# Kernel optimization log

Hardware: AMD Instinct MI355X
Metric: run time of the kernel (lower is better)

The kernel has to match this reference:

```python
import jax, jax.numpy as jnp
import numpy as np

N, H, W, C = 8, 64, 64, 256  # C//4 = 64 query channels, HW = 4096 attention size


def setup_inputs() -> dict:
    key = jax.random.key(0)
    k1, k2, k3, k4 = jax.random.split(key, 4)
    src_mask = jax.random.uniform(k1, (N, H, W), dtype=jnp.float32)
    src_feature = jax.random.normal(k2, (N, H, W, C), dtype=jnp.float32)
    ref_feature = jax.random.normal(k3, (N, H, W, C), dtype=jnp.float32)
    w_query = jax.random.normal(k4, (C, C // 4), dtype=jnp.float32) * 0.02  # 1x1 conv weight
    return {"src_mask": src_mask, "src_feature": src_feature,
            "ref_feature": ref_feature, "w_query": w_query}


def _apply_attention_map(att_map, features):
    n, h, w, c = features.shape
    pixels = features.reshape(n, h * w, c).transpose(0, 2, 1)  # (N, C, HW)
    att_out = jnp.einsum('ncp,npq->ncq', pixels, att_map)      # (N, C, HW)
    return att_out.reshape(n, h, w, c)


def reference(src_mask, src_feature, ref_feature, w_query):
    n, h, w, c = src_feature.shape
    # 1x1 conv (no bias): per-pixel channel projection C -> C//4
    query = jnp.einsum('nhwc,cd->nhwd', src_feature, w_query).reshape(n, h * w, -1)
    # full (HW x HW) attention map, softmax over keys
    att_map = jax.nn.softmax(jnp.einsum('npd,nqd->npq', query, query), axis=-1)
    # original module applies the map to src_feature twice (src_att and ref_att)
    att_out = _apply_attention_map(att_map, src_feature)
    src_att = att_out
    ref_att = att_out
    m = src_mask[..., None]  # (N, H, W, 1)
    ex_guide_flow = m * ref_att + (1.0 - m) * ref_feature
    return jnp.concatenate([ex_guide_flow, src_att], axis=-1)  # (N, H, W, 2C)
```

## Files before the change

### kernel.cpp

```cpp
#include <hip/hip_runtime.h>

typedef unsigned short u16;
typedef unsigned int u32;
typedef __attribute__((ext_vector_type(8))) __bf16 bf16x8;
typedef __attribute__((ext_vector_type(8))) _Float16 f16x8;
typedef __attribute__((ext_vector_type(4))) float f32x4;

__device__ __forceinline__ float b2f(u16 b) {
    union { u32 u; float f; } v; v.u = ((u32)b) << 16; return v.f;
}
__device__ __forceinline__ u16 f2bf(float f) {
    union { float f; u32 u; } v; v.f = f;
    u32 u = v.u;
    return (u16)((u + 0x7fffu + ((u >> 16) & 1u)) >> 16);
}
__device__ __forceinline__ u16 f2h(float f) {
    _Float16 h = (_Float16)f;
    return __builtin_bit_cast(u16, h);
}
__device__ __forceinline__ bf16x8 ldg8b(const u16* p) {
    uint4 v = *(const uint4*)p;
    return __builtin_bit_cast(bf16x8, v);
}
__device__ __forceinline__ f16x8 ldg8h(const u16* p) {
    uint4 v = *(const uint4*)p;
    return __builtin_bit_cast(f16x8, v);
}
__device__ __forceinline__ f32x4 mfma_bf(bf16x8 a, bf16x8 b, f32x4 c) {
    return __builtin_amdgcn_mfma_f32_16x16x32_bf16(a, b, c, 0, 0, 0);
}
__device__ __forceinline__ f32x4 mfma_h(f16x8 a, f16x8 b, f32x4 c) {
    return __builtin_amdgcn_mfma_f32_16x16x32_f16(a, b, c, 0, 0, 0);
}
__device__ __forceinline__ void gld16(const u16* g, u16* l) {
    __builtin_amdgcn_global_load_lds(
        (const __attribute__((address_space(1))) u32*)g,
        (__attribute__((address_space(3))) u32*)l, 16, 0, 0);
}


__global__ void k0_wt(const float* __restrict__ Wq,
                      u16* __restrict__ Wthi, u16* __restrict__ Wtlo) {
    int idx = blockIdx.x * 256 + threadIdx.x;
    int c = idx >> 6, d = idx & 63;
    float w = Wq[idx];
    u16 hi = f2bf(w);
    float rem = w - b2f(hi);
    Wthi[d * 256 + c] = hi;
    Wtlo[d * 256 + c] = f2bf(rem);
}

__global__ __launch_bounds__(256) void k1_query(
    const float* __restrict__ F, const u16* __restrict__ Wthi,
    const u16* __restrict__ Wtlo, u16* __restrict__ Qh) {
    const int t = threadIdx.x;
    const int w = t >> 6, L = t & 63, lane16 = L & 15, quad = L >> 4;
    const int R0 = blockIdx.x * 64;
    const int row = R0 + w * 16 + lane16;
    const f32x4 z4 = {0.f, 0.f, 0.f, 0.f};
    f32x4 acc[4] = {z4, z4, z4, z4};
    union U8 { bf16x8 v; u16 s[8]; };
#pragma unroll
    for (int ks = 0; ks < 8; ++ks) {
        const float* fp = F + (size_t)row * 256 + ks * 32 + quad * 8;
        float4 x0 = *(const float4*)fp;
        float4 x1 = *(const float4*)(fp + 4);
        float xs[8] = {x0.x, x0.y, x0.z, x0.w, x1.x, x1.y, x1.z, x1.w};
        U8 ahi, alo;
#pragma unroll
        for (int j = 0; j < 8; ++j) {
            u16 h = f2bf(xs[j]);
            ahi.s[j] = h;
            alo.s[j] = f2bf(xs[j] - b2f(h));
        }
#pragma unroll
        for (int nt = 0; nt < 4; ++nt) {
            const int off = (nt * 16 + lane16) * 256 + ks * 32 + quad * 8;
            bf16x8 bh = ldg8b(Wthi + off);
            bf16x8 bl = ldg8b(Wtlo + off);
            acc[nt] = mfma_bf(ahi.v, bh, acc[nt]);
            acc[nt] = mfma_bf(alo.v, bh, acc[nt]);
            acc[nt] = mfma_bf(ahi.v, bl, acc[nt]);
        }
    }
    const int orow = R0 + w * 16 + quad * 4;
#pragma unroll
    for (int nt = 0; nt < 4; ++nt) {
        const int d = nt * 16 + lane16;
#pragma unroll
        for (int r = 0; r < 4; ++r) {
            const int p = orow + r;
            Qh[(size_t)p * 64 + (d ^ ((p & 7) << 3))] = f2h(acc[nt][r]);
        }
    }
}

__global__ __launch_bounds__(256) void k2_suminv(
    const u16* __restrict__ Q, float* __restrict__ inv_l) {
    const int t = threadIdx.x;
    const int w = t >> 6, L = t & 63, lane16 = L & 15, quad = L >> 4, l7 = lane16 & 7;
    const int bx = blockIdx.x;
    const int n = bx & 7, pb = bx >> 3;
    const int P0 = pb * 32;
    const u16* Qn = Q + (size_t)n * 4096 * 64;

    f16x8 ap[2][2];
#pragma unroll
    for (int st = 0; st < 2; ++st) {
        const int row = P0 + st * 16 + lane16;
        ap[st][0] = ldg8h(Qn + row * 64 + ((quad * 8) ^ (l7 * 8)));
        ap[st][1] = ldg8h(Qn + row * 64 + ((32 + quad * 8) ^ (l7 * 8)));
    }
    float sums[2][4];
#pragma unroll
    for (int st = 0; st < 2; ++st)
#pragma unroll
        for (int r = 0; r < 4; ++r) sums[st][r] = 0.f;

    const f32x4 z4 = {0.f, 0.f, 0.f, 0.f};
    for (int s = 0; s < 32; ++s) {
#pragma unroll
        for (int nt = 0; nt < 2; ++nt) {
            const int qr = w * 1024 + s * 32 + nt * 16 + lane16;
            f16x8 b0 = ldg8h(Qn + qr * 64 + ((quad * 8) ^ (l7 * 8)));
            f16x8 b1 = ldg8h(Qn + qr * 64 + ((32 + quad * 8) ^ (l7 * 8)));
#pragma unroll
            for (int st = 0; st < 2; ++st) {
                f32x4 z = z4;
                z = mfma_h(ap[st][0], b0, z);
                z = mfma_h(ap[st][1], b1, z);
                sums[st][0] += __expf(z[0]);
                sums[st][1] += __expf(z[1]);
                sums[st][2] += __expf(z[2]);
                sums[st][3] += __expf(z[3]);
            }
        }
    }
    __shared__ float red[4][32];
#pragma unroll
    for (int st = 0; st < 2; ++st)
#pragma unroll
        for (int r = 0; r < 4; ++r) {
            float v = sums[st][r];
            v += __shfl_xor(v, 1);
            v += __shfl_xor(v, 2);
            v += __shfl_xor(v, 4);
            v += __shfl_xor(v, 8);
            if (lane16 == 0) red[w][st * 16 + quad * 4 + r] = v;
        }
    __syncthreads();
    if (t < 32) {
        float tot = red[0][t] + red[1][t] + red[2][t] + red[3][t];
        inv_l[n * 4096 + P0 + t] = 1.0f / tot;
    }
}

__global__ __launch_bounds__(256) void k3_gt(
    const float* __restrict__ F, u16* __restrict__ Gt) {
    const int t = threadIdx.x;
    const int bx = blockIdx.x;
    const int n = bx >> 6, s = bx & 63;
    const int p0 = s * 64;
    __shared__ float tile[64][65];
    const float* Fn = F + (size_t)n * 4096 * 256;
    u16* Gn = Gt + (size_t)(n * 64 + s) * 16384;
#pragma unroll 1
    for (int ct = 0; ct < 4; ++ct) {
        const int c0 = ct * 64;
        if (ct > 0) __syncthreads();
#pragma unroll
        for (int k = 0; k < 16; ++k) {
            int idx = k * 256 + t;
            int r = idx >> 6, cc = idx & 63;
            tile[r][cc] = Fn[(size_t)(p0 + r) * 256 + c0 + cc];
        }
        __syncthreads();
#pragma unroll
        for (int k = 0; k < 2; ++k) {
            int u = k * 256 + t;
            int cc = u & 63, S = u >> 6;
            int G = S ^ (cc & 7);
            u16 v[8];
#pragma unroll
            for (int j = 0; j < 8; ++j) v[j] = f2bf(tile[G * 8 + j][cc]);
            uint4 pk;
            pk.x = (u32)v[0] | ((u32)v[1] << 16);
            pk.y = (u32)v[2] | ((u32)v[3] << 16);
            pk.z = (u32)v[4] | ((u32)v[5] << 16);
            pk.w = (u32)v[6] | ((u32)v[7] << 16);
            *(uint4*)&Gn[(c0 + cc) * 64 + S * 8] = pk;
        }
    }
}

__global__ __launch_bounds__(256, 2) void k4_attn(
    const u16* __restrict__ Q, const u16* __restrict__ Gt,
    const float* __restrict__ invl, const float* __restrict__ mask,
    const float* __restrict__ ref, float* __restrict__ out) {
    const int t = threadIdx.x;
    const int w = t >> 6, L = t & 63, lane16 = L & 15, quad = L >> 4, l7 = lane16 & 7;
    const int bx = blockIdx.x;
    const int n = bx & 7, qb = bx >> 3;
    const int q0 = qb << 6;

    __shared__ u16 sGt[16384];
    __shared__ u16 sQp[4096];
    __shared__ u16 sP[4096];

    const u16* Qn = Q + (size_t)n * 4096 * 64;
    const u16* Gtn = Gt + (size_t)n * 64 * 16384;
    const float* iln = invl + n * 4096;

    f16x8 bq[4][2];
#pragma unroll
    for (int qt = 0; qt < 4; ++qt) {
        const int row = q0 + qt * 16 + lane16;
        bq[qt][0] = ldg8h(Qn + row * 64 + ((quad * 8) ^ (l7 * 8)));
        bq[qt][1] = ldg8h(Qn + row * 64 + ((32 + quad * 8) ^ (l7 * 8)));
    }

    const int pl = w * 16 + lane16;
    const int sA0 = pl * 64 + ((quad * 8) ^ (l7 * 8));
    const int sA1 = pl * 64 + ((32 + quad * 8) ^ (l7 * 8));
    int wrP[4];
#pragma unroll
    for (int qt = 0; qt < 4; ++qt)
        wrP[qt] = (qt * 16 + lane16) * 64 +
                  ((w * 16 + 8 * (quad >> 1)) ^ (l7 * 8)) + 4 * (quad & 1);
    const int dl = L * 8;

    const f32x4 z4 = {0.f, 0.f, 0.f, 0.f};
    f32x4 acc[4][4];
#pragma unroll
    for (int a = 0; a < 4; ++a)
#pragma unroll
        for (int b = 0; b < 4; ++b) acc[a][b] = z4;

#pragma unroll
    for (int j = 0; j < 2; ++j) {
        const int c = w * 2 + j;
        gld16(Qn + c * 512 + dl, &sQp[c * 512]);
    }
    __syncthreads();

#pragma unroll 1
    for (int i = 0; i < 64; ++i) {
#pragma unroll
        for (int j = 0; j < 8; ++j) {
            const int c = w * 8 + j;
            gld16(Gtn + (size_t)i * 16384 + c * 512 + dl, &sGt[c * 512]);
        }
        {
            f16x8 a0 = ldg8h(&sQp[sA0]);
            f16x8 a1 = ldg8h(&sQp[sA1]);
            float4 il4 = *(const float4*)(iln + i * 64 + w * 16 + quad * 4);
#pragma unroll
            for (int qt = 0; qt < 4; ++qt) {
                f32x4 z = z4;
                z = mfma_h(a0, bq[qt][0], z);
                z = mfma_h(a1, bq[qt][1], z);
                ushort4 pk;
                pk.x = f2bf(__expf(z[0]) * il4.x);
                pk.y = f2bf(__expf(z[1]) * il4.y);
                pk.z = f2bf(__expf(z[2]) * il4.z);
                pk.w = f2bf(__expf(z[3]) * il4.w);
                *(ushort4*)&sP[wrP[qt]] = pk;
            }
        }
        __syncthreads();
        if (i + 1 < 64) {
#pragma unroll
            for (int j = 0; j < 2; ++j) {
                const int c = w * 2 + j;
                gld16(Qn + (size_t)(i + 1) * 4096 + c * 512 + dl, &sQp[c * 512]);
            }
        }
#pragma unroll
        for (int h = 0; h < 2; ++h) {
            bf16x8 af[4], bb[4];
#pragma unroll
            for (int m = 0; m < 4; ++m)
                af[m] = ldg8b(&sP[(m * 16 + lane16) * 64 + ((h * 32 + quad * 8) ^ (l7 * 8))]);
#pragma unroll
            for (int nt = 0; nt < 4; ++nt)
                bb[nt] = ldg8b(&sGt[(w * 64 + nt * 16 + lane16) * 64 +
                                    ((h * 32 + quad * 8) ^ (l7 * 8))]);
#pragma unroll
            for (int nt = 0; nt < 4; ++nt)
#pragma unroll
                for (int m = 0; m < 4; ++m)
                    acc[m][nt] = mfma_bf(af[m], bb[nt], acc[m][nt]);
        }
        __syncthreads();
    }

    const int tb = qb >> 2;
    const int cb = (qb & 3) * 64;
    const float* maskn = mask + n * 4096;
    const float* refn = ref + (size_t)n * 4096 * 256;
    float* outn = out + (size_t)n * 4096 * 512;
#pragma unroll
    for (int nt = 0; nt < 4; ++nt) {
        const int ch = w * 64 + nt * 16 + lane16;
        const int pixel = ch * 16 + tb;
        const float m = maskn[pixel];
#pragma unroll
        for (int mt = 0; mt < 4; ++mt) {
            const int c4 = cb + mt * 16 + quad * 4;
            float4 r4 = *(const float4*)(refn + (size_t)pixel * 256 + c4);
            float a0 = acc[mt][nt][0], a1 = acc[mt][nt][1];
            float a2 = acc[mt][nt][2], a3 = acc[mt][nt][3];
            float4 a4 = {a0, a1, a2, a3};
            float4 bl4 = {m * a0 + (1.f - m) * r4.x,
                          m * a1 + (1.f - m) * r4.y,
                          m * a2 + (1.f - m) * r4.z,
                          m * a3 + (1.f - m) * r4.w};
            *(float4*)(outn + (size_t)pixel * 512 + 256 + c4) = a4;
            *(float4*)(outn + (size_t)pixel * 512 + c4) = bl4;
        }
    }
}

extern "C" void kernel_launch(void* const* d_in, const int* in_sizes, int n_in,
                              void* d_out, int out_size, void* d_ws, size_t ws_size,
                              hipStream_t stream) {
    const float* mask = (const float*)d_in[0];
    const float* F    = (const float*)d_in[1];
    const float* ref  = (const float*)d_in[2];
    const float* Wq   = (const float*)d_in[3];
    float* out = (float*)d_out;
    char* ws = (char*)d_ws;

    u16*   Wthi = (u16*)ws;
    u16*   Wtlo = (u16*)(ws + 32768);
    u16*   Qh   = (u16*)(ws + 65536);
    float* invl = (float*)(ws + 65536 + 4194304);
    u16*   Gt   = (u16*)(ws + 65536 + 4194304 + 131072);

    k0_wt    <<<64,   256, 0, stream>>>(Wq, Wthi, Wtlo);
    k1_query <<<512,  256, 0, stream>>>(F, Wthi, Wtlo, Qh);
    k2_suminv<<<1024, 256, 0, stream>>>(Qh, invl);
    k3_gt    <<<512,  256, 0, stream>>>(F, Gt);
    k4_attn  <<<512,  256, 0, stream>>>(Qh, Gt, invl, mask, ref, out);
}
```

Measured before the change: 272.1 us.

## Load Gt and Q fragments directly into registers, double-buffer P in LDS

The attention kernel stops staging the Gt and Q tiles through shared memory with global_load_lds. Each wave now loads its own Gt B-fragments and the next step's Q A-fragments and inverse-sum values straight into registers, prefetching one step ahead. The P tile is double-buffered in LDS, so each iteration needs one barrier instead of two. This cuts LDS traffic and occupancy pressure but raises register use and exposes global-load latency on the Gt fragments, which are issued in the same iteration that consumes them.

```diff
diff --git a/kernel.cpp b/kernel.cpp
--- a/kernel.cpp
+++ b/kernel.cpp
@@ -31,11 +31,6 @@
 }
 __device__ __forceinline__ f32x4 mfma_h(f16x8 a, f16x8 b, f32x4 c) {
     return __builtin_amdgcn_mfma_f32_16x16x32_f16(a, b, c, 0, 0, 0);
-}
-__device__ __forceinline__ void gld16(const u16* g, u16* l) {
-    __builtin_amdgcn_global_load_lds(
-        (const __attribute__((address_space(1))) u32*)g,
-        (__attribute__((address_space(3))) u32*)l, 16, 0, 0);
 }
 
 
@@ -203,31 +198,31 @@
     const int n = bx & 7, qb = bx >> 3;
     const int q0 = qb << 6;
 
-    __shared__ u16 sGt[16384];
-    __shared__ u16 sQp[4096];
-    __shared__ u16 sP[4096];
+    __shared__ u16 sP[2][4096];
 
     const u16* Qn = Q + (size_t)n * 4096 * 64;
     const u16* Gtn = Gt + (size_t)n * 64 * 16384;
     const float* iln = invl + n * 4096;
 
+    const int o0 = (quad * 8) ^ (l7 * 8);
+
     f16x8 bq[4][2];
 #pragma unroll
     for (int qt = 0; qt < 4; ++qt) {
-        const int row = q0 + qt * 16 + lane16;
-        bq[qt][0] = ldg8h(Qn + row * 64 + ((quad * 8) ^ (l7 * 8)));
-        bq[qt][1] = ldg8h(Qn + row * 64 + ((32 + quad * 8) ^ (l7 * 8)));
-    }
-
-    const int pl = w * 16 + lane16;
-    const int sA0 = pl * 64 + ((quad * 8) ^ (l7 * 8));
-    const int sA1 = pl * 64 + ((32 + quad * 8) ^ (l7 * 8));
+        const u16* r = Qn + (q0 + qt * 16 + lane16) * 64;
+        bq[qt][0] = ldg8h(r + o0);
+        bq[qt][1] = ldg8h(r + (o0 ^ 32));
+    }
+
+    const u16* qrow = Qn + (w * 16 + lane16) * 64;
+    const u16* grow = Gtn + (w * 64 + lane16) * 64;
+    const float* ilp = iln + w * 16 + quad * 4;
+
     int wrP[4];
 #pragma unroll
     for (int qt = 0; qt < 4; ++qt)
         wrP[qt] = (qt * 16 + lane16) * 64 +
                   ((w * 16 + 8 * (quad >> 1)) ^ (l7 * 8)) + 4 * (quad & 1);
-    const int dl = L * 8;
 
     const f32x4 z4 = {0.f, 0.f, 0.f, 0.f};
     f32x4 acc[4][4];
@@ -236,63 +231,71 @@
 #pragma unroll
         for (int b = 0; b < 4; ++b) acc[a][b] = z4;
 
-#pragma unroll
-    for (int j = 0; j < 2; ++j) {
-        const int c = w * 2 + j;
-        gld16(Qn + c * 512 + dl, &sQp[c * 512]);
-    }
-    __syncthreads();
+    f16x8 qa0[2], qa1[2];
+    float4 il[2];
+    bf16x8 gb[8];
+
+#define LOADSTEP(slot, step) do {                       \
+        const u16* _q = qrow + (step) * 4096;           \
+        qa0[slot] = ldg8h(_q + o0);                     \
+        qa1[slot] = ldg8h(_q + (o0 ^ 32));              \
+        il[slot] = *(const float4*)(ilp + (step) * 64); \
+    } while (0)
+
+#define LOADGB(step) do {                                   \
+        const u16* _g = grow + (size_t)(step) * 16384;      \
+        _Pragma("unroll")                                   \
+        for (int nt = 0; nt < 4; ++nt) {                    \
+            gb[nt * 2 + 0] = ldg8b(_g + nt * 1024 + o0);    \
+            gb[nt * 2 + 1] = ldg8b(_g + nt * 1024 + (o0 ^ 32)); \
+        }                                                   \
+    } while (0)
+
+#define ITER(i, cur, nxt) do {                                        \
+        LOADGB(i);                                                    \
+        if ((i) + 1 < 64) LOADSTEP(nxt, (i) + 1);                     \
+        {                   \
+            f16x8 a0 = qa0[cur], a1 = qa1[cur];                       \
+            float4 il4 = il[cur];                                     \
+            _Pragma("unroll")                                         \
+            for (int qt = 0; qt < 4; ++qt) {                          \
+                f32x4 z = z4;                                         \
+                z = mfma_h(a0, bq[qt][0], z);                         \
+                z = mfma_h(a1, bq[qt][1], z);                         \
+                ushort4 pk;                                           \
+                pk.x = f2bf(__expf(z[0]) * il4.x);                    \
+                pk.y = f2bf(__expf(z[1]) * il4.y);                    \
+                pk.z = f2bf(__expf(z[2]) * il4.z);                    \
+                pk.w = f2bf(__expf(z[3]) * il4.w);                    \
+                *(ushort4*)&sP[(i) & 1][wrP[qt]] = pk;                \
+            }                                                         \
+        }                                                             \
+        asm volatile("s_waitcnt lgkmcnt(0)\n\ts_barrier" ::: "memory"); \
+        _Pragma("unroll")                                             \
+        for (int h = 0; h < 2; ++h) {                   \
+            bf16x8 af[4];                                             \
+            _Pragma("unroll")                                         \
+            for (int m = 0; m < 4; ++m)                               \
+                af[m] = ldg8b(&sP[(i) & 1][(m * 16 + lane16) * 64 + (o0 ^ (h * 32))]); \
+            _Pragma("unroll")                                         \
+            for (int nt = 0; nt < 4; ++nt) {                          \
+                _Pragma("unroll")                                     \
+                for (int m = 0; m < 4; ++m)                           \
+                    acc[m][nt] = mfma_bf(af[m], gb[nt * 2 + h], acc[m][nt]); \
+            }                                                         \
+        }                                                             \
+    } while (0)
+
+    LOADSTEP(0, 0);
 
 #pragma unroll 1
-    for (int i = 0; i < 64; ++i) {
-#pragma unroll
-        for (int j = 0; j < 8; ++j) {
-            const int c = w * 8 + j;
-            gld16(Gtn + (size_t)i * 16384 + c * 512 + dl, &sGt[c * 512]);
-        }
-        {
-            f16x8 a0 = ldg8h(&sQp[sA0]);
-            f16x8 a1 = ldg8h(&sQp[sA1]);
-            float4 il4 = *(const float4*)(iln + i * 64 + w * 16 + quad * 4);
-#pragma unroll
-            for (int qt = 0; qt < 4; ++qt) {
-                f32x4 z = z4;
-                z = mfma_h(a0, bq[qt][0], z);
-                z = mfma_h(a1, bq[qt][1], z);
-                ushort4 pk;
-                pk.x = f2bf(__expf(z[0]) * il4.x);
-                pk.y = f2bf(__expf(z[1]) * il4.y);
-                pk.z = f2bf(__expf(z[2]) * il4.z);
-                pk.w = f2bf(__expf(z[3]) * il4.w);
-                *(ushort4*)&sP[wrP[qt]] = pk;
-            }
-        }
-        __syncthreads();
-        if (i + 1 < 64) {
-#pragma unroll
-            for (int j = 0; j < 2; ++j) {
-                const int c = w * 2 + j;
-                gld16(Qn + (size_t)(i + 1) * 4096 + c * 512 + dl, &sQp[c * 512]);
-            }
-        }
-#pragma unroll
-        for (int h = 0; h < 2; ++h) {
-            bf16x8 af[4], bb[4];
-#pragma unroll
-            for (int m = 0; m < 4; ++m)
-                af[m] = ldg8b(&sP[(m * 16 + lane16) * 64 + ((h * 32 + quad * 8) ^ (l7 * 8))]);
-#pragma unroll
-            for (int nt = 0; nt < 4; ++nt)
-                bb[nt] = ldg8b(&sGt[(w * 64 + nt * 16 + lane16) * 64 +
-                                    ((h * 32 + quad * 8) ^ (l7 * 8))]);
-#pragma unroll
-            for (int nt = 0; nt < 4; ++nt)
-#pragma unroll
-                for (int m = 0; m < 4; ++m)
-                    acc[m][nt] = mfma_bf(af[m], bb[nt], acc[m][nt]);
-        }
-        __syncthreads();
-    }
+    for (int ii = 0; ii < 32; ++ii) {
+        ITER(2 * ii, 0, 1);
+        ITER(2 * ii + 1, 1, 0);
+    }
+#undef ITER
+#undef LOADGB
+#undef LOADSTEP
 
     const int tb = qb >> 2;
     const int cb = (qb & 3) * 64;
```

After: 277.5 us. +2.0%, slower.
